# Kernel optimization log

Measured on AMD Instinct MI355X. Metric: run time of the kernel, lower is better.

Reference implementation:

```python
import jax, jax.numpy as jnp
import numpy as np

N, E, D, H, C = 100000, 1600000, 128, 256, 40


def setup_inputs() -> dict:
    key = jax.random.key(0)
    ks = jax.random.split(key, 10)
    x = jax.random.normal(ks[0], (N, D), dtype=jnp.float32)
    src = jax.random.randint(ks[1], (E,), 0, N, dtype=jnp.int32)
    dst = jax.random.randint(ks[2], (E,), 0, N, dtype=jnp.int32)
    # GIN layer 1 MLP (bias-free), kaiming-uniform-like scale 1/sqrt(fan_in)
    w1a = jax.random.normal(ks[3], (D, H), dtype=jnp.float32) / np.sqrt(D)
    w1b = jax.random.normal(ks[4], (H, H), dtype=jnp.float32) / np.sqrt(H)
    # GIN layer 2 MLP
    w2a = jax.random.normal(ks[5], (H, H), dtype=jnp.float32) / np.sqrt(H)
    w2b = jax.random.normal(ks[6], (H, H), dtype=jnp.float32) / np.sqrt(H)
    # eps initialized to 0 per reset_parameters
    eps1 = jnp.zeros((), dtype=jnp.float32)
    eps2 = jnp.zeros((), dtype=jnp.float32)
    # final classifier fc (with bias)
    fc_w = jax.random.normal(ks[7], (H, C), dtype=jnp.float32) / np.sqrt(H)
    fc_b = jax.random.normal(ks[8], (C,), dtype=jnp.float32) * 0.01
    return {"x": x, "src": src, "dst": dst,
            "eps1": eps1, "w1a": w1a, "w1b": w1b,
            "eps2": eps2, "w2a": w2a, "w2b": w2b,
            "fc_w": fc_w, "fc_b": fc_b}


def reference(x, src, dst, eps1, w1a, w1b, eps2, w2a, w2b, fc_w, fc_b):
    n = x.shape[0]

    def gin_layer(h, eps, wa, wb):
        # GINConv sum-aggregation: scatter-add neighbor feats over edges
        agg = jax.ops.segment_sum(h[src], dst, num_segments=n)  # [N, d]
        rst = (1.0 + eps) * h + agg
        # 2-layer bias-free MLP with ReLU between
        return jax.nn.relu(rst @ wa) @ wb

    h = jax.nn.relu(gin_layer(x, eps1, w1a, w1b))   # layer + outer activation
    h = jax.nn.relu(gin_layer(h, eps2, w2a, w2b))   # dropout p=0 -> identity
    return h @ fc_w + fc_b                           # [N, C]
```

## Files before the change

### kernel.cpp

```cpp
#include <hip/hip_runtime.h>

#define N_NODES 100000
#define N_EDGES 1600000
#define DIM_IN  128
#define DIM_H   256
#define DIM_C   40

#define NB   391
#define NBLK 391
#define CHUNK 4096
#define ECAP 6144

#define CVT_BLOCKS 25000
#define WCVT_BLOCKS 1280

typedef unsigned short bf16_t;
typedef __attribute__((ext_vector_type(8))) short short8;
typedef __attribute__((ext_vector_type(4))) float f32x4;

__device__ __forceinline__ bf16_t f2b(float f) {
    unsigned int u = __float_as_uint(f);
    unsigned int r = (u + 0x7fffu + ((u >> 16) & 1u)) >> 16;
    return (bf16_t)r;
}

__device__ __forceinline__ void gl_lds16(const void* gsrc, void* ldst) {
    __builtin_amdgcn_global_load_lds(
        (const __attribute__((address_space(1))) void*)gsrc,
        (__attribute__((address_space(3))) void*)ldst,
        16, 0, 0);
}


__global__ __launch_bounds__(256) void k_prep(
    const int* __restrict__ dst, int* __restrict__ cnt2,
    const float* __restrict__ x, signed char* __restrict__ x8, float* __restrict__ xs,
    const float* __restrict__ w1a, const float* __restrict__ w1b,
    const float* __restrict__ w2a, const float* __restrict__ w2b,
    const float* __restrict__ fcw,
    bf16_t* __restrict__ o1a, bf16_t* __restrict__ o1b,
    bf16_t* __restrict__ o2a, bf16_t* __restrict__ o2b, bf16_t* __restrict__ ofc,
    int* __restrict__ ticket)
{
    __shared__ int h[NB];
    int blk = blockIdx.x, t = threadIdx.x;

    if (blk < NBLK) {
        if (blk == 0 && t == 0) *ticket = 0;
        for (int i = t; i < NB; i += 256) h[i] = 0;
        __syncthreads();
        int base = blk * CHUNK;
        int end = min(base + CHUNK, N_EDGES);
        for (int i = base + t; i < end; i += 256)
            atomicAdd(&h[dst[i] >> 8], 1);
        __syncthreads();
        for (int i = t; i < NB; i += 256) cnt2[blk * NB + i] = h[i];
        return;
    }
    blk -= NBLK;

    if (blk < CVT_BLOCKS) {
        int gid = blk * 256 + t;
        int u = gid >> 6, lane = gid & 63;
        float2 v = *(const float2*)(x + (size_t)u * 128 + lane * 2);
        float m = fmaxf(fabsf(v.x), fabsf(v.y));
        #pragma unroll
        for (int d = 1; d < 64; d <<= 1)
            m = fmaxf(m, __shfl_xor(m, d, 64));
        float inv = (m > 0.f) ? 127.f / m : 0.f;
        int q0 = (int)rintf(v.x * inv);
        int q1 = (int)rintf(v.y * inv);
        unsigned short pk = (unsigned short)((q0 & 0xff) | ((q1 & 0xff) << 8));
        *(unsigned short*)(x8 + ((unsigned)u << 7) + lane * 2) = pk;
        if (lane == 0) xs[u] = (m > 0.f) ? m * (1.f / 127.f) : 0.f;
        return;
    }
    blk -= CVT_BLOCKS;

    int r = blk >> 8;
    int idx = (blk & 255) * 256 + t;
    const float* in; bf16_t* out; int K, N, Npad;
    switch (r) {
        case 0: in = w1a; out = o1a; K = 128; N = 256; Npad = 256; break;
        case 1: in = w1b; out = o1b; K = 256; N = 256; Npad = 256; break;
        case 2: in = w2a; out = o2a; K = 256; N = 256; Npad = 256; break;
        case 3: in = w2b; out = o2b; K = 256; N = 256; Npad = 256; break;
        default: in = fcw; out = ofc; K = 256; N = 40;  Npad = 64;  break;
    }
    if (idx >= Npad * K) return;
    int n = idx / K, k = idx - n * K;
    float v = (n < N) ? in[(size_t)k * N + n] : 0.f;
    int kstep = k >> 5, quad = (k >> 3) & 3, e = k & 7;
    int tt = n >> 4, l15 = n & 15;
    size_t opos = (size_t)kstep * (Npad * 32) + ((tt * 4 + quad) * 16 + l15) * 8 + e;
    out[opos] = f2b(v);
}


__global__ void k_bscanA(const int* __restrict__ cnt2, int* __restrict__ basep,
                         int* __restrict__ btot, int* __restrict__ ticket,
                         int* __restrict__ boff) {
    __shared__ int s[512];
    __shared__ int isLast;
    int t = threadIdx.x, b = blockIdx.x;
    int v = (t < NBLK) ? cnt2[t * NB + b] : 0;
    s[t] = v;
    __syncthreads();
    #pragma unroll
    for (int d = 1; d < 512; d <<= 1) {
        int tv = (t >= d) ? s[t - d] : 0;
        __syncthreads();
        s[t] += tv;
        __syncthreads();
    }
    if (t < NBLK) basep[t * NB + b] = s[t] - v;
    if (t == 511) atomicExch(&btot[b], s[511]);
    __syncthreads();
    if (t == 0) {
        __threadfence();
        int old = atomicAdd(ticket, 1);
        isLast = (old == NB - 1);
    }
    __syncthreads();
    if (!isLast) return;

    __threadfence();
    int v2 = (t < NB) ? atomicAdd(&btot[t], 0) : 0;
    s[t] = v2;
    __syncthreads();
    #pragma unroll
    for (int d = 1; d < 512; d <<= 1) {
        int tv = (t >= d) ? s[t - d] : 0;
        __syncthreads();
        s[t] += tv;
        __syncthreads();
    }
    if (t < NB) boff[t] = s[t] - v2;
    if (t == NB - 1) boff[NB] = s[t];
}

__global__ void k_bscatter(const int* __restrict__ src, const int* __restrict__ dst,
                           const int* __restrict__ basep, const int* __restrict__ boff,
                           int* __restrict__ ebuf, int e) {
    __shared__ int cur[NB];
    int t = threadIdx.x, blk = blockIdx.x;
    for (int i = t; i < NB; i += 256) cur[i] = basep[blk * NB + i] + boff[i];
    __syncthreads();
    int base = blk * CHUNK;
    int end = min(base + CHUNK, e);
    for (int i = base + t; i < end; i += 256) {
        int sv = src[i], dv = dst[i];
        int pos = atomicAdd(&cur[dv >> 8], 1);
        ebuf[pos] = sv | ((dv & 255) << 24);
    }
}

__global__ __launch_bounds__(256) void k_build(const int* __restrict__ ebuf,
                                               const int* __restrict__ boff,
                                               int* __restrict__ off,
                                               int* __restrict__ csr) {
    __shared__ int ec[ECAP];
    __shared__ int h[256];
    __shared__ int cur[256];
    int t = threadIdx.x, b = blockIdx.x;
    int node0 = b << 8;
    int e0 = boff[b], e1 = boff[b + 1];
    int ne = e1 - e0;
    bool fits = (ne <= ECAP);
    h[t] = 0;
    __syncthreads();
    if (fits) {
        for (int i = t; i < ne; i += 256) {
            int p = ebuf[e0 + i];
            ec[i] = p;
            atomicAdd(&h[(unsigned)p >> 24], 1);
        }
    } else {
        for (int i = t; i < ne; i += 256)
            atomicAdd(&h[(unsigned)ebuf[e0 + i] >> 24], 1);
    }
    __syncthreads();
    int mydeg = h[t];
    #pragma unroll
    for (int d = 1; d < 256; d <<= 1) {
        int tv = (t >= d) ? h[t - d] : 0;
        __syncthreads();
        h[t] += tv;
        __syncthreads();
    }
    int node = node0 + t;
    if (node < N_NODES) off[node + 1] = e0 + h[t];
    if (b == 0 && t == 0) off[0] = 0;
    cur[t] = e0 + h[t] - mydeg;
    __syncthreads();
    if (fits) {
        for (int i = t; i < ne; i += 256) {
            int p = ec[i];
            int pos = atomicAdd(&cur[(unsigned)p >> 24], 1);
            csr[pos] = p & 0xFFFFFF;
        }
    } else {
        for (int i = t; i < ne; i += 256) {
            int p = ebuf[e0 + i];
            int pos = atomicAdd(&cur[(unsigned)p >> 24], 1);
            csr[pos] = p & 0xFFFFFF;
        }
    }
}


__global__ void k_agg_i8(const signed char* __restrict__ h8, const float* __restrict__ hs,
                         const int* __restrict__ off, const int* __restrict__ csr,
                         const float* __restrict__ eps_p,
                         bf16_t* __restrict__ rst, int n) {
    int gid = blockIdx.x * blockDim.x + threadIdx.x;
    int u = __builtin_amdgcn_readfirstlane(gid >> 6);
    int lane = threadIdx.x & 63;
    if (u >= n) return;

    float acc0 = 0.f, acc1 = 0.f;
    int r0 = off[u], r1 = off[u + 1];
    unsigned loff = lane * 2u;

    for (int base = r0; base < r1; base += 64) {
        int m = r1 - base; if (m > 64) m = 64;
        int li = (lane < m) ? lane : (m - 1);
        int iv = csr[base + li];
        for (int c = 0; c < m; c += 16) {
            int s[16]; float sc[16]; unsigned v[16];
            #pragma unroll
            for (int t = 0; t < 16; t++)
                s[t] = __builtin_amdgcn_readlane(iv, c + t);
            #pragma unroll
            for (int t = 0; t < 16; t++)
                sc[t] = (c + t < m) ? hs[s[t]] : 0.f;
            #pragma unroll
            for (int t = 0; t < 16; t++)
                v[t] = *(const unsigned short*)(h8 + (((unsigned)s[t] << 7) + loff));
            #pragma unroll
            for (int t = 0; t < 16; t++) {
                acc0 += (float)(int)(signed char)(v[t] & 0xffu) * sc[t];
                acc1 += (float)(int)(signed char)(v[t] >> 8) * sc[t];
            }
        }
    }

    float scu = hs[u] * (1.0f + eps_p[0]);
    unsigned vu = *(const unsigned short*)(h8 + (((unsigned)u << 7) + loff));
    float o0 = (float)(int)(signed char)(vu & 0xffu) * scu + acc0;
    float o1 = (float)(int)(signed char)(vu >> 8) * scu + acc1;
    *(unsigned int*)(rst + ((unsigned)u << 7) + lane * 2) =
        (unsigned int)f2b(o0) | ((unsigned int)f2b(o1) << 16);
}


__global__ void k_agg_u8(const unsigned char* __restrict__ h8,
                         const float* __restrict__ hs,
                         const int* __restrict__ off, const int* __restrict__ csr,
                         const float* __restrict__ eps_p,
                         bf16_t* __restrict__ rst, int n) {
    int gid = blockIdx.x * blockDim.x + threadIdx.x;
    int u = __builtin_amdgcn_readfirstlane(gid >> 6);
    int lane = threadIdx.x & 63;
    if (u >= n) return;

    float acc[4] = {0.f, 0.f, 0.f, 0.f};
    int r0 = off[u], r1 = off[u + 1];
    unsigned loff = lane * 4u;

    for (int base = r0; base < r1; base += 64) {
        int m = r1 - base; if (m > 64) m = 64;
        int li = (lane < m) ? lane : (m - 1);
        int iv = csr[base + li];
        for (int c = 0; c < m; c += 16) {
            int s[16]; float sc[16]; unsigned int v[16];
            #pragma unroll
            for (int t = 0; t < 16; t++)
                s[t] = __builtin_amdgcn_readlane(iv, c + t);
            #pragma unroll
            for (int t = 0; t < 16; t++)
                sc[t] = (c + t < m) ? hs[s[t]] : 0.f;
            #pragma unroll
            for (int t = 0; t < 16; t++)
                v[t] = *(const unsigned int*)(h8 + (((unsigned)s[t] << 8) + loff));
            #pragma unroll
            for (int t = 0; t < 16; t++) {
                acc[0] += (float)(v[t] & 0xffu) * sc[t];
                acc[1] += (float)((v[t] >> 8) & 0xffu) * sc[t];
                acc[2] += (float)((v[t] >> 16) & 0xffu) * sc[t];
                acc[3] += (float)(v[t] >> 24) * sc[t];
            }
        }
    }

    float ep = 1.0f + eps_p[0];
    unsigned int vu = *(const unsigned int*)(h8 + (((unsigned)u << 8) + loff));
    float scu = hs[u] * ep;
    float o0 = (float)(vu & 0xffu) * scu + acc[0];
    float o1 = (float)((vu >> 8) & 0xffu) * scu + acc[1];
    float o2 = (float)((vu >> 16) & 0xffu) * scu + acc[2];
    float o3 = (float)(vu >> 24) * scu + acc[3];
    uint2 ov;
    ov.x = (unsigned int)f2b(o0) | ((unsigned int)f2b(o1) << 16);
    ov.y = (unsigned int)f2b(o2) | ((unsigned int)f2b(o3) << 16);
    *(uint2*)(rst + (size_t)u * 256 + lane * 4) = ov;
}


#define TS_STRIDE 264

template <int K1, bool OUT8, bool FUSE_FC>
__global__ __launch_bounds__(256, 2) void k_mlp(
    const bf16_t* __restrict__ A, const bf16_t* __restrict__ W1t,
    const bf16_t* __restrict__ W2t, bf16_t* __restrict__ H,
    unsigned char* __restrict__ H8, float* __restrict__ Hs,
    const bf16_t* __restrict__ FCt, const float* __restrict__ fc_b,
    float* __restrict__ Cout, int M)
{
    __shared__ __align__(16) bf16_t Bs[2][256 * 32];
    __shared__ __align__(16) bf16_t Ts[64 * TS_STRIDE];
    __shared__ int rmax[64];

    int tid = threadIdx.x;
    int wave = tid >> 6, lane = tid & 63;
    int l15 = lane & 15, quad = lane >> 4;
    int bm = blockIdx.x * 64;

    auto stageB = [&](const bf16_t* W, int kstep, int b) {
        #pragma unroll
        for (int l = 0; l < 4; l++) {
            int c = l * 256 + tid;
            gl_lds16(W + ((size_t)kstep * 1024 + c) * 8, &Bs[b][c * 8]);
        }
    };

    f32x4 acc[4][4];
    #pragma unroll
    for (int i = 0; i < 4; i++)
        #pragma unroll
        for (int j = 0; j < 4; j++) acc[i][j] = 0.f;

    constexpr int NS1 = K1 / 32;
    short8 afr[NS1][4];
    #pragma unroll
    for (int ks = 0; ks < NS1; ks++)
        #pragma unroll
        for (int i = 0; i < 4; i++) {
            int gr = bm + i * 16 + l15; if (gr >= M) gr = M - 1;
            afr[ks][i] = *(const short8*)(A + (size_t)gr * K1 + ks * 32 + quad * 8);
        }

    stageB(W1t, 0, 0);
    #pragma unroll
    for (int k = 0; k < NS1; k++) {
        int cur = k & 1;
        if (k + 1 < NS1) {
            stageB(W1t, k + 1, cur ^ 1);
            asm volatile("s_waitcnt vmcnt(4)" ::: "memory");
        } else {
            asm volatile("s_waitcnt vmcnt(0)" ::: "memory");
        }
        __builtin_amdgcn_sched_barrier(0);
        __builtin_amdgcn_s_barrier();

        short8 bfv[4];
        #pragma unroll
        for (int j = 0; j < 4; j++)
            bfv[j] = *(const short8*)&Bs[cur][((wave * 4 + j) * 64 + lane) * 8];

        #pragma unroll
        for (int i = 0; i < 4; i++)
            #pragma unroll
            for (int j = 0; j < 4; j++)
                acc[i][j] = __builtin_amdgcn_mfma_f32_16x16x32_bf16(afr[k][i], bfv[j], acc[i][j], 0, 0, 0);

        asm volatile("s_waitcnt lgkmcnt(0)" ::: "memory");
        __builtin_amdgcn_sched_barrier(0);
        __builtin_amdgcn_s_barrier();
    }

    int wn = wave * 64;
    #pragma unroll
    for (int i = 0; i < 4; i++)
        #pragma unroll
        for (int j = 0; j < 4; j++) {
            int row = i * 16 + quad * 4;
            int col = wn + j * 16 + l15;
            #pragma unroll
            for (int r = 0; r < 4; r++)
                Ts[(row + r) * TS_STRIDE + col] = f2b(fmaxf(acc[i][j][r], 0.f));
        }

    #pragma unroll
    for (int i = 0; i < 4; i++)
        #pragma unroll
        for (int j = 0; j < 4; j++) acc[i][j] = 0.f;
    __syncthreads();

    stageB(W2t, 0, 0);
    #pragma unroll
    for (int k = 0; k < 8; k++) {
        int cur = k & 1;
        if (k + 1 < 8) {
            stageB(W2t, k + 1, cur ^ 1);
            asm volatile("s_waitcnt vmcnt(4)" ::: "memory");
        } else {
            asm volatile("s_waitcnt vmcnt(0)" ::: "memory");
        }
        __builtin_amdgcn_sched_barrier(0);
        __builtin_amdgcn_s_barrier();

        short8 af[4], bfv[4];
        #pragma unroll
        for (int i = 0; i < 4; i++)
            af[i] = *(const short8*)&Ts[(i * 16 + l15) * TS_STRIDE + k * 32 + quad * 8];
        #pragma unroll
        for (int j = 0; j < 4; j++)
            bfv[j] = *(const short8*)&Bs[cur][((wave * 4 + j) * 64 + lane) * 8];

        #pragma unroll
        for (int i = 0; i < 4; i++)
            #pragma unroll
            for (int j = 0; j < 4; j++)
                acc[i][j] = __builtin_amdgcn_mfma_f32_16x16x32_bf16(af[i], bfv[j], acc[i][j], 0, 0, 0);

        asm volatile("s_waitcnt lgkmcnt(0)" ::: "memory");
        __builtin_amdgcn_sched_barrier(0);
        __builtin_amdgcn_s_barrier();
    }

    if constexpr (OUT8) {
        if (tid < 64) rmax[tid] = 0;
        __syncthreads();
        #pragma unroll
        for (int i = 0; i < 4; i++)
            #pragma unroll
            for (int r = 0; r < 4; r++) {
                float m = 0.f;
                #pragma unroll
                for (int j = 0; j < 4; j++) m = fmaxf(m, acc[i][j][r]);
                atomicMax(&rmax[i * 16 + quad * 4 + r], __float_as_int(m));
            }
        __syncthreads();
        #pragma unroll
        for (int i = 0; i < 4; i++) {
            #pragma unroll
            for (int r = 0; r < 4; r++) {
                int row = i * 16 + quad * 4 + r;
                int rowg = bm + row;
                if (rowg >= M) continue;
                float rm = __int_as_float(rmax[row]);
                float inv = (rm > 0.f) ? 255.f / rm : 0.f;
                #pragma unroll
                for (int j = 0; j < 4; j++) {
                    int col = wn + j * 16 + l15;
                    float v = fmaxf(acc[i][j][r], 0.f);
                    unsigned q = (unsigned)(v * inv + 0.5f);
                    if (q > 255u) q = 255u;
                    H8[(size_t)rowg * 256 + col] = (unsigned char)q;
                }
                if (wave == 0 && l15 == 0)
                    Hs[rowg] = rm * (1.f / 255.f);
            }
        }
    } else if constexpr (FUSE_FC) {
        #pragma unroll
        for (int i = 0; i < 4; i++)
            #pragma unroll
            for (int j = 0; j < 4; j++) {
                int row = i * 16 + quad * 4;
                int col = wn + j * 16 + l15;
                #pragma unroll
                for (int r = 0; r < 4; r++)
                    Ts[(row + r) * TS_STRIDE + col] = f2b(fmaxf(acc[i][j][r], 0.f));
            }
        __syncthreads();

        f32x4 acc3[3];
        #pragma unroll
        for (int j = 0; j < 3; j++) acc3[j] = 0.f;

        auto stage3 = [&](int kstep, int b) {
            gl_lds16(FCt + ((size_t)kstep * 256 + tid) * 8, &Bs[b][tid * 8]);
        };

        stage3(0, 0);
        #pragma unroll
        for (int k = 0; k < 8; k++) {
            int cur = k & 1;
            if (k + 1 < 8) {
                stage3(k + 1, cur ^ 1);
                asm volatile("s_waitcnt vmcnt(1)" ::: "memory");
            } else {
                asm volatile("s_waitcnt vmcnt(0)" ::: "memory");
            }
            __builtin_amdgcn_sched_barrier(0);
            __builtin_amdgcn_s_barrier();

            short8 af = *(const short8*)&Ts[(wave * 16 + l15) * TS_STRIDE + k * 32 + quad * 8];
            #pragma unroll
            for (int j = 0; j < 3; j++) {
                short8 bfv = *(const short8*)&Bs[cur][((j * 64) + lane) * 8];
                acc3[j] = __builtin_amdgcn_mfma_f32_16x16x32_bf16(af, bfv, acc3[j], 0, 0, 0);
            }

            asm volatile("s_waitcnt lgkmcnt(0)" ::: "memory");
            __builtin_amdgcn_sched_barrier(0);
            __builtin_amdgcn_s_barrier();
        }

        #pragma unroll
        for (int j = 0; j < 3; j++) {
            int col = j * 16 + l15;
            if (col >= DIM_C) continue;
            float bv = fc_b[col];
            #pragma unroll
            for (int r = 0; r < 4; r++) {
                int rowg = bm + wave * 16 + quad * 4 + r;
                if (rowg < M)
                    Cout[(size_t)rowg * DIM_C + col] = acc3[j][r] + bv;
            }
        }
    } else {
        #pragma unroll
        for (int j = 0; j < 4; j++) {
            int col = wn + j * 16 + l15;
            #pragma unroll
            for (int i = 0; i < 4; i++) {
                #pragma unroll
                for (int r = 0; r < 4; r++) {
                    int rowg = bm + i * 16 + quad * 4 + r;
                    if (rowg < M)
                        H[(size_t)rowg * 256 + col] = f2b(fmaxf(acc[i][j][r], 0.f));
                }
            }
        }
    }
}


static inline size_t rnd256(size_t x) { return (x + 255) & ~(size_t)255; }

extern "C" void kernel_launch(void* const* d_in, const int* in_sizes, int n_in,
                              void* d_out, int out_size, void* d_ws, size_t ws_size,
                              hipStream_t stream) {
    const float* x    = (const float*)d_in[0];
    const int*   src  = (const int*)d_in[1];
    const int*   dst  = (const int*)d_in[2];
    const float* eps1 = (const float*)d_in[3];
    const float* w1a  = (const float*)d_in[4];
    const float* w1b  = (const float*)d_in[5];
    const float* eps2 = (const float*)d_in[6];
    const float* w2a  = (const float*)d_in[7];
    const float* w2b  = (const float*)d_in[8];
    const float* fc_w = (const float*)d_in[9];
    const float* fc_b = (const float*)d_in[10];
    float* out = (float*)d_out;

    char* w = (char*)d_ws;
    int* off  = (int*)w; w += rnd256(sizeof(int) * (size_t)(N_NODES + 1));
    int* csr  = (int*)w; w += rnd256(sizeof(int) * (size_t)N_EDGES);
    int* cnt2  = (int*)w; w += rnd256(sizeof(int) * (size_t)NBLK * NB);
    int* basep = (int*)w; w += rnd256(sizeof(int) * (size_t)NBLK * NB);
    int* btot  = (int*)w; w += rnd256(sizeof(int) * 512);
    int* boff  = (int*)w; w += rnd256(sizeof(int) * (NB + 1));
    bf16_t* w1a_t = (bf16_t*)w; w += rnd256(2 * (size_t)DIM_H * DIM_IN);
    bf16_t* w1b_t = (bf16_t*)w; w += rnd256(2 * (size_t)DIM_H * DIM_H);
    bf16_t* w2a_t = (bf16_t*)w; w += rnd256(2 * (size_t)DIM_H * DIM_H);
    bf16_t* w2b_t = (bf16_t*)w; w += rnd256(2 * (size_t)DIM_H * DIM_H);
    bf16_t* fc_t  = (bf16_t*)w; w += rnd256(2 * (size_t)128 * DIM_H);
    signed char* x8 = (signed char*)w; w += rnd256((size_t)N_NODES * DIM_IN);
    float* xs = (float*)w; w += rnd256(sizeof(float) * (size_t)N_NODES);
    unsigned char* h8 = (unsigned char*)w; w += rnd256((size_t)N_NODES * DIM_H);
    float* hs = (float*)w; w += rnd256(sizeof(float) * (size_t)N_NODES);
    bf16_t* R12 = (bf16_t*)w; w += rnd256(2 * (size_t)N_NODES * DIM_H);
    bf16_t* R3  = (bf16_t*)w; w += rnd256(2 * (size_t)N_NODES * DIM_H);

    bf16_t* rst1 = R12;
    int* ebuf = (int*)R3;
    int* ticket = btot + 500;

    k_prep<<<NBLK + CVT_BLOCKS + WCVT_BLOCKS, 256, 0, stream>>>(
        dst, cnt2, x, x8, xs, w1a, w1b, w2a, w2b, fc_w,
        w1a_t, w1b_t, w2a_t, w2b_t, fc_t, ticket);

    k_bscanA<<<NB, 512, 0, stream>>>(cnt2, basep, btot, ticket, boff);
    k_bscatter<<<NBLK, 256, 0, stream>>>(src, dst, basep, boff, ebuf, N_EDGES);
    k_build<<<NB, 256, 0, stream>>>(ebuf, boff, off, csr);

    const int agg_blocks = (N_NODES * 64 + 255) / 256;
    const int mlp_blocks = (N_NODES + 63) / 64;

    k_agg_i8<<<agg_blocks, 256, 0, stream>>>(x8, xs, off, csr, eps1, rst1, N_NODES);
    k_mlp<DIM_IN, true, false><<<mlp_blocks, 256, 0, stream>>>(
        rst1, w1a_t, w1b_t, nullptr, h8, hs, nullptr, nullptr, nullptr, N_NODES);

    k_agg_u8<<<agg_blocks, 256, 0, stream>>>(h8, hs, off, csr, eps2, (bf16_t*)R3, N_NODES);
    k_mlp<DIM_H, false, true><<<mlp_blocks, 256, 0, stream>>>(
        (bf16_t*)R3, w2a_t, w2b_t, nullptr, nullptr, nullptr, fc_t, fc_b, out, N_NODES);
}
```

Baseline: 429.1 us.

## Write aggregation output in MFMA-fragment tiled layout and stream A tiles through LDS

```diff
diff --git a/kernel.cpp b/kernel.cpp
--- a/kernel.cpp
+++ b/kernel.cpp
@@ -1,6 +1,7 @@
 #include <hip/hip_runtime.h>
 
 #define N_NODES 100000
+#define NPAD    100032
 #define N_EDGES 1600000
 #define DIM_IN  128
 #define DIM_H   256
@@ -92,7 +93,7 @@
     float v = (n < N) ? in[(size_t)k * N + n] : 0.f;
     int kstep = k >> 5, quad = (k >> 3) & 3, e = k & 7;
     int tt = n >> 4, l15 = n & 15;
-    size_t opos = (size_t)kstep * (Npad * 32) + ((tt * 4 + quad) * 16 + l15) * 8 + e;
+    size_t opos = (size_t)kstep * (Npad * 32) + ((size_t)(tt * 64 + quad * 16 + l15)) * 8 + e;
     out[opos] = f2b(v);
 }
 
@@ -249,7 +250,12 @@
     unsigned vu = *(const unsigned short*)(h8 + (((unsigned)u << 7) + loff));
     float o0 = (float)(int)(signed char)(vu & 0xffu) * scu + acc0;
     float o1 = (float)(int)(signed char)(vu >> 8) * scu + acc1;
-    *(unsigned int*)(rst + ((unsigned)u << 7) + lane * 2) =
+
+    int R = u >> 6, rr = u & 63;
+    int i4 = rr >> 4, l15v = rr & 15;
+    int ks = lane >> 4, quad = (lane >> 2) & 3, e2 = (lane & 3) * 2;
+    size_t pos = (((size_t)R * 4 + ks) * 256 + (size_t)(i4 * 64 + quad * 16 + l15v)) * 8 + e2;
+    *(unsigned int*)(rst + pos) =
         (unsigned int)f2b(o0) | ((unsigned int)f2b(o1) << 16);
 }
 
@@ -303,7 +309,12 @@
     uint2 ov;
     ov.x = (unsigned int)f2b(o0) | ((unsigned int)f2b(o1) << 16);
     ov.y = (unsigned int)f2b(o2) | ((unsigned int)f2b(o3) << 16);
-    *(uint2*)(rst + (size_t)u * 256 + lane * 4) = ov;
+
+    int R = u >> 6, rr = u & 63;
+    int i4 = rr >> 4, l15v = rr & 15;
+    int ks = lane >> 3, quad = (lane >> 1) & 3, e4 = (lane & 1) * 4;
+    size_t pos = (((size_t)R * 8 + ks) * 256 + (size_t)(i4 * 64 + quad * 16 + l15v)) * 8 + e4;
+    *(uint2*)(rst + pos) = ov;
 }
 
 
@@ -317,6 +328,8 @@
     const bf16_t* __restrict__ FCt, const float* __restrict__ fc_b,
     float* __restrict__ Cout, int M)
 {
+    constexpr int NS1 = K1 / 32;
+    __shared__ __align__(16) bf16_t As[2][64 * 32];
     __shared__ __align__(16) bf16_t Bs[2][256 * 32];
     __shared__ __align__(16) bf16_t Ts[64 * TS_STRIDE];
     __shared__ int rmax[64];
@@ -326,6 +339,9 @@
     int l15 = lane & 15, quad = lane >> 4;
     int bm = blockIdx.x * 64;
 
+    auto stageA = [&](int kstep, int b) {
+        gl_lds16(A + ((size_t)blockIdx.x * NS1 + kstep) * 2048 + tid * 8, &As[b][tid * 8]);
+    };
     auto stageB = [&](const bf16_t* W, int kstep, int b) {
         #pragma unroll
         for (int l = 0; l < 4; l++) {
@@ -340,30 +356,23 @@
         #pragma unroll
         for (int j = 0; j < 4; j++) acc[i][j] = 0.f;
 
-    constexpr int NS1 = K1 / 32;
-    short8 afr[NS1][4];
-    #pragma unroll
-    for (int ks = 0; ks < NS1; ks++)
-        #pragma unroll
-        for (int i = 0; i < 4; i++) {
-            int gr = bm + i * 16 + l15; if (gr >= M) gr = M - 1;
-            afr[ks][i] = *(const short8*)(A + (size_t)gr * K1 + ks * 32 + quad * 8);
-        }
-
-    stageB(W1t, 0, 0);
+    stageA(0, 0); stageB(W1t, 0, 0);
     #pragma unroll
     for (int k = 0; k < NS1; k++) {
         int cur = k & 1;
         if (k + 1 < NS1) {
-            stageB(W1t, k + 1, cur ^ 1);
-            asm volatile("s_waitcnt vmcnt(4)" ::: "memory");
+            stageA(k + 1, cur ^ 1); stageB(W1t, k + 1, cur ^ 1);
+            asm volatile("s_waitcnt vmcnt(5)" ::: "memory");
         } else {
             asm volatile("s_waitcnt vmcnt(0)" ::: "memory");
         }
         __builtin_amdgcn_sched_barrier(0);
         __builtin_amdgcn_s_barrier();
 
-        short8 bfv[4];
+        short8 af[4], bfv[4];
+        #pragma unroll
+        for (int i = 0; i < 4; i++)
+            af[i] = *(const short8*)&As[cur][(i * 64 + lane) * 8];
         #pragma unroll
         for (int j = 0; j < 4; j++)
             bfv[j] = *(const short8*)&Bs[cur][((wave * 4 + j) * 64 + lane) * 8];
@@ -372,7 +381,7 @@
         for (int i = 0; i < 4; i++)
             #pragma unroll
             for (int j = 0; j < 4; j++)
-                acc[i][j] = __builtin_amdgcn_mfma_f32_16x16x32_bf16(afr[k][i], bfv[j], acc[i][j], 0, 0, 0);
+                acc[i][j] = __builtin_amdgcn_mfma_f32_16x16x32_bf16(af[i], bfv[j], acc[i][j], 0, 0, 0);
 
         asm volatile("s_waitcnt lgkmcnt(0)" ::: "memory");
         __builtin_amdgcn_sched_barrier(0);
@@ -573,8 +582,8 @@
     float* xs = (float*)w; w += rnd256(sizeof(float) * (size_t)N_NODES);
     unsigned char* h8 = (unsigned char*)w; w += rnd256((size_t)N_NODES * DIM_H);
     float* hs = (float*)w; w += rnd256(sizeof(float) * (size_t)N_NODES);
-    bf16_t* R12 = (bf16_t*)w; w += rnd256(2 * (size_t)N_NODES * DIM_H);
-    bf16_t* R3  = (bf16_t*)w; w += rnd256(2 * (size_t)N_NODES * DIM_H);
+    bf16_t* R12 = (bf16_t*)w; w += rnd256(2 * (size_t)NPAD * DIM_H);
+    bf16_t* R3  = (bf16_t*)w; w += rnd256(2 * (size_t)NPAD * DIM_H);
 
     bf16_t* rst1 = R12;
     int* ebuf = (int*)R3;
@@ -589,7 +598,7 @@
     k_build<<<NB, 256, 0, stream>>>(ebuf, boff, off, csr);
 
     const int agg_blocks = (N_NODES * 64 + 255) / 256;
-    const int mlp_blocks = (N_NODES + 63) / 64;
+    const int mlp_blocks = NPAD / 64;
 
     k_agg_i8<<<agg_blocks, 256, 0, stream>>>(x8, xs, off, csr, eps1, rst1, N_NODES);
     k_mlp<DIM_IN, true, false><<<mlp_blocks, 256, 0, stream>>>(
```

Result: faster. 410.8 us (-4.3%).
